# Kernel tuning notes

Measured on AMD Instinct MI355X. Metric: run time of the kernel, lower is better.

Reference implementation:

```python
import jax, jax.numpy as jnp
import numpy as np

# Production-scale sampled 2-hop GraphSAGE flow
N, C, HID, OUT = 1_000_000, 128, 32, 16
NSRC1, NDST1, E1 = 600_000, 80_000, 1_280_000
NDST2, E2 = 8_000, 80_000


def setup_inputs() -> dict:
    key = jax.random.key(0)
    ks = jax.random.split(key, 8)
    x = jax.random.normal(ks[0], (N, C), jnp.float32)
    n_id = jax.random.randint(ks[1], (NSRC1,), 0, N)
    src1 = jax.random.randint(ks[2], (E1,), 0, NSRC1)
    dst1 = jax.random.randint(ks[3], (E1,), 0, NDST1)
    src2 = jax.random.randint(ks[4], (E2,), 0, NDST1)
    dst2 = jax.random.randint(ks[5], (E2,), 0, NDST2)
    W1 = jax.random.normal(ks[6], (C, HID), jnp.float32) / np.sqrt(C).astype(np.float32)
    b1 = jnp.zeros((HID,), jnp.float32)
    W2 = jax.random.normal(ks[7], (HID, OUT), jnp.float32) / np.sqrt(HID).astype(np.float32)
    b2 = jnp.zeros((OUT,), jnp.float32)
    return dict(x=x, n_id=n_id, src1=src1, dst1=dst1, src2=src2, dst2=dst2,
                W1=W1, b1=b1, W2=W2, b2=b2)


def _mean_agg(feat_src, src, dst, num_dst):
    # scatter-mean of source features onto destination nodes (PyG aggr='mean')
    msg = feat_src[src]                                          # [E, F]
    s = jax.ops.segment_sum(msg, dst, num_segments=num_dst)      # [num_dst, F]
    cnt = jax.ops.segment_sum(jnp.ones((src.shape[0],), feat_src.dtype), dst,
                              num_segments=num_dst)
    return s / jnp.maximum(cnt, 1.0)[:, None]


def reference(x, n_id, src1, dst1, src2, dst2, W1, b1, W2, b2):
    h = x[n_id]                                  # gather sampled nodes [NSRC1, C]
    # SAGEConv(concat=False, normalize=False): mean-agg then linear
    h = _mean_agg(h, src1, dst1, NDST1) @ W1 + b1
    h = jax.nn.relu(h)                           # F.dropout(p=0.5) is a no-op in eval
    h = _mean_agg(h, src2, dst2, NDST2) @ W2 + b2
    return jax.nn.log_softmax(h, axis=1)
```

## Files before the change

### kernel.cpp

```cpp
#include <hip/hip_runtime.h>
#include <hip/hip_fp16.h>
#include <math.h>

#define N_NODES  1000000
#define C_IN     128
#define HID      32
#define OUTF     16
#define NSRC1    600000
#define NDST1    80000
#define E1       1280000
#define NDST2    8000
#define E2       80000

#define KB1 4688
#define HB1 5000
#define HB2 313
#define AB1 313
#define AB2 32

#define K1_STRIDE 36

__global__ __launch_bounds__(256) void kA_transform_hist(
    const float* __restrict__ x, const int* __restrict__ n_id,
    const float* __restrict__ W1, __half* __restrict__ p,
    const int* __restrict__ dst1, const int* __restrict__ dst2,
    int* __restrict__ deg1, int* __restrict__ deg2)
{
    __shared__ float W_s[C_IN * HID];
    __shared__ float A_t[4][32 * K1_STRIDE];

    const int bid = blockIdx.x;
    int role, idx;
    if (bid < 2 * KB1) { role = bid & 1; idx = bid >> 1; }
    else {
        int r = bid - 2 * KB1;
        if (r < HB1 - KB1) { role = 1; idx = KB1 + r; }
        else               { role = 2; idx = r - (HB1 - KB1); }
    }

    if (role == 1) {
        int e = idx * 256 + threadIdx.x;
        if (e < E1) atomicAdd(&deg1[dst1[e]], 1);
        return;
    }
    if (role == 2) {
        int e = idx * 256 + threadIdx.x;
        if (e < E2) atomicAdd(&deg2[dst2[e]], 1);
        return;
    }

    for (int i = threadIdx.x; i < C_IN * HID; i += 256) W_s[i] = W1[i];
    __syncthreads();

    const int wave = threadIdx.x >> 6;
    const int lane = threadIdx.x & 63;
    const int gwave = idx * 4 + wave;
    if (gwave >= NSRC1 / 32) return;
    const int s0 = gwave * 32;

    float* At = A_t[wave];

    int   mrow[4]; int f8[4]; const float* rowp[4];
    #pragma unroll
    for (int j = 0; j < 4; ++j) {
        int i2 = j * 64 + lane;
        mrow[j] = i2 >> 3;
        f8[j]   = i2 & 7;
        rowp[j] = x + (size_t)n_id[s0 + mrow[j]] * C_IN + f8[j] * 4;
    }

    const int m4 = lane >> 3;
    const int o4 = lane & 7;

    float acc[4][4];
    #pragma unroll
    for (int i = 0; i < 4; ++i)
        #pragma unroll
        for (int j = 0; j < 4; ++j) acc[i][j] = 0.f;

    float4 v[4];
    #pragma unroll
    for (int j = 0; j < 4; ++j) v[j] = *(const float4*)(rowp[j]);

    #pragma unroll
    for (int c = 0; c < 4; ++c) {
        #pragma unroll
        for (int j = 0; j < 4; ++j) {
            int kb = f8[j] * 4;
            int m  = mrow[j];
            At[(kb + 0) * K1_STRIDE + m] = v[j].x;
            At[(kb + 1) * K1_STRIDE + m] = v[j].y;
            At[(kb + 2) * K1_STRIDE + m] = v[j].z;
            At[(kb + 3) * K1_STRIDE + m] = v[j].w;
        }
        if (c < 3) {
            #pragma unroll
            for (int j = 0; j < 4; ++j)
                v[j] = *(const float4*)(rowp[j] + (c + 1) * 32);
        }
        #pragma unroll 4
        for (int k = 0; k < 32; ++k) {
            float4 a = *(const float4*)&At[k * K1_STRIDE + m4 * 4];
            float4 w = *(const float4*)&W_s[(c * 32 + k) * HID + o4 * 4];
            acc[0][0] += a.x * w.x; acc[0][1] += a.x * w.y; acc[0][2] += a.x * w.z; acc[0][3] += a.x * w.w;
            acc[1][0] += a.y * w.x; acc[1][1] += a.y * w.y; acc[1][2] += a.y * w.z; acc[1][3] += a.y * w.w;
            acc[2][0] += a.z * w.x; acc[2][1] += a.z * w.y; acc[2][2] += a.z * w.z; acc[2][3] += a.z * w.w;
            acc[3][0] += a.w * w.x; acc[3][1] += a.w * w.y; acc[3][2] += a.w * w.z; acc[3][3] += a.w * w.w;
        }
    }

    #pragma unroll
    for (int i = 0; i < 4; ++i) {
        union { __half2 h2[2]; uint2 u; } pk;
        pk.h2[0] = __floats2half2_rn(acc[i][0], acc[i][1]);
        pk.h2[1] = __floats2half2_rn(acc[i][2], acc[i][3]);
        *(uint2*)&p[(size_t)(s0 + m4 * 4 + i) * HID + o4 * 4] = pk.u;
    }
}

__global__ __launch_bounds__(256) void kB_alloc(
    const int* __restrict__ deg1, const int* __restrict__ deg2,
    int* __restrict__ rs1, int* __restrict__ rs2,
    int* __restrict__ cur1, int* __restrict__ cur2,
    int* __restrict__ counters)
{
    const int bid  = blockIdx.x;
    const int lane = threadIdx.x & 63;
    const int* deg; int* rs; int* cur; int* ctr; int nd; int d;
    if (bid < AB1) { deg = deg1; rs = rs1; cur = cur1; ctr = counters + 0;
                     nd = NDST1; d = bid * 256 + threadIdx.x; }
    else           { deg = deg2; rs = rs2; cur = cur2; ctr = counters + 1;
                     nd = NDST2; d = (bid - AB1) * 256 + threadIdx.x; }

    int v = (d < nd) ? deg[d] : 0;
    int incl = v;
    #pragma unroll
    for (int off = 1; off < 64; off <<= 1) {
        int t = __shfl_up(incl, off, 64);
        if (lane >= off) incl += t;
    }
    int total = __shfl(incl, 63, 64);
    int base = 0;
    if (lane == 63) base = atomicAdd(ctr, total);
    base = __shfl(base, 63, 64);
    if (d < nd) { int r = base + incl - v; rs[d] = r; cur[d] = r; }
}

__global__ __launch_bounds__(256) void kC_bucket(
    const int* __restrict__ src1, const int* __restrict__ dst1,
    const int* __restrict__ src2, const int* __restrict__ dst2,
    int* __restrict__ cur1, int* __restrict__ cur2,
    int* __restrict__ ss1, int* __restrict__ ss2)
{
    const int bid = blockIdx.x;
    if (bid < HB1) {
        int e = bid * 256 + threadIdx.x;
        if (e < E1) {
            int d = dst1[e];
            int pos = atomicAdd(&cur1[d], 1);
            ss1[pos] = src1[e];
        }
    } else {
        int e = (bid - HB1) * 256 + threadIdx.x;
        if (e < E2) {
            int d = dst2[e];
            int pos = atomicAdd(&cur2[d], 1);
            ss2[pos] = src2[e];
        }
    }
}

__global__ __launch_bounds__(256) void kD_gather1(
    const int* __restrict__ row_start, const int* __restrict__ deg,
    const int* __restrict__ ss1, const __half* __restrict__ p,
    const float* __restrict__ b1, const float* __restrict__ W2,
    float* __restrict__ q)
{
    __shared__ float hbuf[16][HID + 1];
    const int g = threadIdx.x >> 4;
    const int f = threadIdx.x & 15;
    const int d = blockIdx.x * 16 + g;

    float w2r[HID];
    #pragma unroll
    for (int k = 0; k < HID; ++k) w2r[k] = W2[k * OUTF + f];
    const float2 b1v = *(const float2*)&b1[2 * f];

    const int start = row_start[d];
    const int dg    = deg[d];
    const __half2* ph2 = (const __half2*)p;

    float2 acc = make_float2(0.f, 0.f);
    int i = 0;
    for (; i + 4 <= dg; i += 4) {
        int s0 = ss1[start + i];
        int s1 = ss1[start + i + 1];
        int s2 = ss1[start + i + 2];
        int s3 = ss1[start + i + 3];
        float2 a = __half22float2(ph2[(size_t)s0 * 16 + f]);
        float2 b = __half22float2(ph2[(size_t)s1 * 16 + f]);
        float2 c = __half22float2(ph2[(size_t)s2 * 16 + f]);
        float2 e = __half22float2(ph2[(size_t)s3 * 16 + f]);
        acc.x += (a.x + b.x) + (c.x + e.x);
        acc.y += (a.y + b.y) + (c.y + e.y);
    }
    for (; i < dg; ++i) {
        float2 a = __half22float2(ph2[(size_t)ss1[start + i] * 16 + f]);
        acc.x += a.x; acc.y += a.y;
    }

    const float inv = 1.f / (float)max(dg, 1);
    hbuf[g][2 * f]     = fmaxf(acc.x * inv + b1v.x, 0.f);
    hbuf[g][2 * f + 1] = fmaxf(acc.y * inv + b1v.y, 0.f);
    float o = 0.f;
    #pragma unroll
    for (int k = 0; k < HID; ++k) o += hbuf[g][k] * w2r[k];
    q[(size_t)d * OUTF + f] = o;
}

__global__ __launch_bounds__(256) void kE_gather2_lsm(
    const int* __restrict__ row_start2, const int* __restrict__ deg2,
    const int* __restrict__ ss2, const float* __restrict__ q,
    const float* __restrict__ b2, float* __restrict__ out)
{
    const int g = threadIdx.x >> 4;
    const int f = threadIdx.x & 15;
    const int d = blockIdx.x * 16 + g;
    if (d >= NDST2) return;

    const int start = row_start2[d];
    const int dg    = deg2[d];

    float acc = 0.f;
    int i = 0;
    for (; i + 2 <= dg; i += 2) {
        int s0 = ss2[start + i];
        int s1 = ss2[start + i + 1];
        acc += q[(size_t)s0 * OUTF + f] + q[(size_t)s1 * OUTF + f];
    }
    if (i < dg) acc += q[(size_t)ss2[start + i] * OUTF + f];

    float z = acc / (float)max(dg, 1) + b2[f];
    float m = z;
    #pragma unroll
    for (int off = 8; off; off >>= 1) m = fmaxf(m, __shfl_xor(m, off, 16));
    float e = expf(z - m);
    float s = e;
    #pragma unroll
    for (int off = 8; off; off >>= 1) s += __shfl_xor(s, off, 16);
    out[(size_t)d * OUTF + f] = z - m - logf(s);
}

extern "C" void kernel_launch(void* const* d_in, const int* in_sizes, int n_in,
                              void* d_out, int out_size, void* d_ws, size_t ws_size,
                              hipStream_t stream)
{
    const float* x    = (const float*)d_in[0];
    const int*   n_id = (const int*)  d_in[1];
    const int*   src1 = (const int*)  d_in[2];
    const int*   dst1 = (const int*)  d_in[3];
    const int*   src2 = (const int*)  d_in[4];
    const int*   dst2 = (const int*)  d_in[5];
    const float* W1   = (const float*)d_in[6];
    const float* b1   = (const float*)d_in[7];
    const float* W2   = (const float*)d_in[8];
    const float* b2   = (const float*)d_in[9];
    float* out = (float*)d_out;

    char* ws = (char*)d_ws;
    __half* p       = (__half*)(ws + 0);
    int*   ss1      = (int*)   (ws + 38400000);
    int*   ss2      = (int*)   (ws + 43520000);
    int*   deg1     = (int*)   (ws + 43840000);
    int*   deg2     = (int*)   (ws + 44160000);
    int*   counters = (int*)   (ws + 44192000);
    int*   rs1      = (int*)   (ws + 44192064);
    int*   rs2      = (int*)   (ws + 44512064);
    int*   cur1     = (int*)   (ws + 44544064);
    int*   cur2     = (int*)   (ws + 44864064);
    float* q        = (float*) (ws + 44896064);

    hipMemsetAsync(deg1, 0, 352064, stream);

    kA_transform_hist<<<2 * KB1 + (HB1 - KB1) + HB2, 256, 0, stream>>>(
        x, n_id, W1, p, dst1, dst2, deg1, deg2);

    kB_alloc <<<AB1 + AB2, 256, 0, stream>>>(deg1, deg2, rs1, rs2, cur1, cur2,
                                             counters);

    kC_bucket<<<HB1 + HB2, 256, 0, stream>>>(src1, dst1, src2, dst2,
                                             cur1, cur2, ss1, ss2);

    kD_gather1<<<NDST1 / 16, 256, 0, stream>>>(rs1, deg1, ss1, p, b1, W2, q);

    kE_gather2_lsm<<<NDST2 / 16, 256, 0, stream>>>(rs2, deg2, ss2, q, b2, out);
}
```

Measured before the change: 808.8 us.

## Split layer-1 transform across histogram and bucket kernels to overlap atomics

The dense gather-and-transform work (x[n_id] @ W1) was previously fused only with the degree histogram. It is now split into two parts: about a quarter of the tiles run interleaved with the histogram blocks, and the rest are co-scheduled with the bucket-scatter kernel. The aim is to hide the latency-bound atomic scatter phases behind bandwidth-heavy transform work in both kernels. In exchange, the bucket kernel now allocates large shared memory in every block, which may lower occupancy for its atomic-only blocks, and the block-index interleaving becomes more complex.

```diff
diff --git a/kernel.cpp b/kernel.cpp
--- a/kernel.cpp
+++ b/kernel.cpp
@@ -18,37 +18,17 @@
 #define AB1 313
 #define AB2 32
 
+#define T1A  1250
+#define T1B  (KB1 - T1A)
+#define GRP2 1719
+
 #define K1_STRIDE 36
 
-__global__ __launch_bounds__(256) void kA_transform_hist(
+__device__ __forceinline__ void transform_body(
     const float* __restrict__ x, const int* __restrict__ n_id,
     const float* __restrict__ W1, __half* __restrict__ p,
-    const int* __restrict__ dst1, const int* __restrict__ dst2,
-    int* __restrict__ deg1, int* __restrict__ deg2)
-{
-    __shared__ float W_s[C_IN * HID];
-    __shared__ float A_t[4][32 * K1_STRIDE];
-
-    const int bid = blockIdx.x;
-    int role, idx;
-    if (bid < 2 * KB1) { role = bid & 1; idx = bid >> 1; }
-    else {
-        int r = bid - 2 * KB1;
-        if (r < HB1 - KB1) { role = 1; idx = KB1 + r; }
-        else               { role = 2; idx = r - (HB1 - KB1); }
-    }
-
-    if (role == 1) {
-        int e = idx * 256 + threadIdx.x;
-        if (e < E1) atomicAdd(&deg1[dst1[e]], 1);
-        return;
-    }
-    if (role == 2) {
-        int e = idx * 256 + threadIdx.x;
-        if (e < E2) atomicAdd(&deg2[dst2[e]], 1);
-        return;
-    }
-
+    float* W_s, float (*A_t)[32 * K1_STRIDE], int idx)
+{
     for (int i = threadIdx.x; i < C_IN * HID; i += 256) W_s[i] = W1[i];
     __syncthreads();
 
@@ -118,6 +98,32 @@
     }
 }
 
+__global__ __launch_bounds__(256) void kA1_hist_transform(
+    const float* __restrict__ x, const int* __restrict__ n_id,
+    const float* __restrict__ W1, __half* __restrict__ p,
+    const int* __restrict__ dst1, const int* __restrict__ dst2,
+    int* __restrict__ deg1, int* __restrict__ deg2)
+{
+    __shared__ float W_s[C_IN * HID];
+    __shared__ float A_t[4][32 * K1_STRIDE];
+
+    const int bid = blockIdx.x;
+    const int t = bid / 5, r = bid % 5;
+    if (r == 0 && t < T1A) {
+        transform_body(x, n_id, W1, p, W_s, A_t, t);
+        return;
+    }
+    const int nt = min((bid + 4) / 5, T1A);
+    const int h  = bid - nt;
+    if (h < HB1) {
+        int e = h * 256 + threadIdx.x;
+        if (e < E1) atomicAdd(&deg1[dst1[e]], 1);
+    } else {
+        int e = (h - HB1) * 256 + threadIdx.x;
+        if (e < E2) atomicAdd(&deg2[dst2[e]], 1);
+    }
+}
+
 __global__ __launch_bounds__(256) void kB_alloc(
     const int* __restrict__ deg1, const int* __restrict__ deg2,
     int* __restrict__ rs1, int* __restrict__ rs2,
@@ -146,22 +152,44 @@
     if (d < nd) { int r = base + incl - v; rs[d] = r; cur[d] = r; }
 }
 
-__global__ __launch_bounds__(256) void kC_bucket(
+__global__ __launch_bounds__(256) void kA2_bucket_transform(
+    const float* __restrict__ x, const int* __restrict__ n_id,
+    const float* __restrict__ W1, __half* __restrict__ p,
     const int* __restrict__ src1, const int* __restrict__ dst1,
     const int* __restrict__ src2, const int* __restrict__ dst2,
     int* __restrict__ cur1, int* __restrict__ cur2,
     int* __restrict__ ss1, int* __restrict__ ss2)
 {
+    __shared__ float W_s[C_IN * HID];
+    __shared__ float A_t[4][32 * K1_STRIDE];
+
     const int bid = blockIdx.x;
-    if (bid < HB1) {
-        int e = bid * 256 + threadIdx.x;
+    const int g = bid / 5, r = bid % 5;
+    int bidx;
+    if (g < GRP2) {
+        if (r < 2) {
+            int ti = 2 * g + r;
+            if (ti < T1B) {
+                transform_body(x, n_id, W1, p, W_s, A_t, T1A + ti);
+                return;
+            }
+            bidx = 0;
+        } else {
+            bidx = 3 * g + (r - 2);
+        }
+    } else {
+        bidx = 3 * GRP2 + (bid - 5 * GRP2);
+    }
+
+    if (bidx < HB1) {
+        int e = bidx * 256 + threadIdx.x;
         if (e < E1) {
             int d = dst1[e];
             int pos = atomicAdd(&cur1[d], 1);
             ss1[pos] = src1[e];
         }
     } else {
-        int e = (bid - HB1) * 256 + threadIdx.x;
+        int e = (bidx - HB1) * 256 + threadIdx.x;
         if (e < E2) {
             int d = dst2[e];
             int pos = atomicAdd(&cur2[d], 1);
@@ -282,14 +310,14 @@
 
     hipMemsetAsync(deg1, 0, 352064, stream);
 
-    kA_transform_hist<<<2 * KB1 + (HB1 - KB1) + HB2, 256, 0, stream>>>(
+    kA1_hist_transform<<<T1A + HB1 + HB2, 256, 0, stream>>>(
         x, n_id, W1, p, dst1, dst2, deg1, deg2);
 
-    kB_alloc <<<AB1 + AB2, 256, 0, stream>>>(deg1, deg2, rs1, rs2, cur1, cur2,
-                                             counters);
-
-    kC_bucket<<<HB1 + HB2, 256, 0, stream>>>(src1, dst1, src2, dst2,
-                                             cur1, cur2, ss1, ss2);
+    kB_alloc<<<AB1 + AB2, 256, 0, stream>>>(deg1, deg2, rs1, rs2, cur1, cur2,
+                                            counters);
+
+    kA2_bucket_transform<<<T1B + HB1 + HB2, 256, 0, stream>>>(
+        x, n_id, W1, p, src1, dst1, src2, dst2, cur1, cur2, ss1, ss2);
 
     kD_gather1<<<NDST1 / 16, 256, 0, stream>>>(rs1, deg1, ss1, p, b1, W2, q);
 
```

Measured after the change: 754.8 us. -6.7%, faster.
